# Kernel optimization log

Hardware: AMD Instinct MI355X
Metric: run time of the kernel (lower is better)

Reference implementation:

```python
import jax, jax.numpy as jnp
import numpy as np

B, Q, D = 8, 128, 2048
H, HD = 16, 128           # num_heads, head_dim (D == H*HD)
CACHE = 3968              # tokens already in KV cache; CACHE+Q == max_seq_len


def setup_inputs() -> dict:
    key = jax.random.key(0)
    ks = jax.random.split(key, 6)
    x = jax.random.normal(ks[0], (B, Q, D), dtype=jnp.float32)
    k_cache = jax.random.normal(ks[1], (B, H, CACHE, HD), dtype=jnp.float32)
    v_cache = jax.random.normal(ks[2], (B, H, CACHE, HD), dtype=jnp.float32)
    Wqkv = jax.random.normal(ks[3], (D, 3 * D), dtype=jnp.float32) * 0.02
    Wproj = jax.random.normal(ks[4], (D, D), dtype=jnp.float32) * 0.02
    bproj = jnp.zeros((D,), dtype=jnp.float32)
    return {"x": x, "k_cache": k_cache, "v_cache": v_cache,
            "Wqkv": Wqkv, "Wproj": Wproj, "bproj": bproj}


def reference(x, k_cache, v_cache, Wqkv, Wproj, bproj):
    # QKV projection (qkv_bias=False)
    qkv = x @ Wqkv                                   # [B, Q, 3D]
    qkv = qkv.reshape(B, Q, 3, H, HD)
    qkv = jnp.transpose(qkv, (2, 0, 3, 1, 4))        # [3, B, H, Q, HD]
    q, k_new, v_new = qkv[0], qkv[1], qkv[2]
    # KV-cache append (cache_pos + Q == max_seq_len, no roll)
    k_all = jnp.concatenate([k_cache, k_new], axis=2)  # [B, H, K, HD]
    v_all = jnp.concatenate([v_cache, v_new], axis=2)
    K = CACHE + Q
    scale = 1.0 / jnp.sqrt(jnp.float32(HD))
    scores = jnp.einsum('bhqd,bhkd->bhqk', q, k_all) * scale  # [B, H, Q, K]
    # Causal mask aligned to cache (bottom-right): query i sees keys j <= i + (K - Q)
    i = jnp.arange(Q)[:, None]
    j = jnp.arange(K)[None, :]
    mask = j > (i + (K - Q))
    scores = jnp.where(mask, jnp.float32(-jnp.inf), scores)
    attn = jax.nn.softmax(scores, axis=-1)
    out = jnp.einsum('bhqk,bhkd->bhqd', attn, v_all)   # [B, H, Q, HD]
    out = jnp.transpose(out, (0, 2, 1, 3)).reshape(B, Q, D)
    return out @ Wproj + bproj
```

## Files before the change

### kernel.cpp

```cpp
#include <hip/hip_runtime.h>

typedef unsigned int u32;
typedef unsigned short u16;
typedef short s16x8 __attribute__((ext_vector_type(8)));
typedef float f32x4 __attribute__((ext_vector_type(4)));

#define MFMA16(a,b,c) __builtin_amdgcn_mfma_f32_16x16x32_bf16((a),(b),(c),0,0,0)

#define Bb 8
#define Hh 16
#define Qq 128
#define HDd 128
#define Dd 2048
#define CACHE 3968
#define NSPLIT 8
#define SCALE 0.08838834764831845f
#define SM_OFF 8.0f

__device__ __forceinline__ u16 f2bf(float x){
  u32 u = __builtin_bit_cast(u32, x);
  u32 r = ((u >> 16) & 1u) + 0x7fffu;
  return (u16)((u + r) >> 16);
}
__device__ __forceinline__ float bf2f(u16 h){
  return __builtin_bit_cast(float, ((u32)h) << 16);
}
__device__ __forceinline__ u32 pk2(float a, float b){
  return (u32)f2bf(a) | ((u32)f2bf(b) << 16);
}
__device__ __forceinline__ u32 cvtpk(float a, float b){
  u32 r;
  asm("v_cvt_pk_bf16_f32 %0, %1, %2" : "=v"(r) : "v"(a), "v"(b));
  return r;
}
__device__ __forceinline__ float f4c(const float4& v, int j){
  return j==0 ? v.x : j==1 ? v.y : j==2 ? v.z : v.w;
}
__device__ __forceinline__ void gload_lds16(const void* g, void* l){
  __builtin_amdgcn_global_load_lds(
      (const __attribute__((address_space(1))) u32*)g,
      (__attribute__((address_space(3))) u32*)l, 16, 0, 0);
}
__device__ __forceinline__ void lgkm_barrier(){
  asm volatile("s_waitcnt lgkmcnt(0)" ::: "memory");
  __builtin_amdgcn_s_barrier();
}

__global__ void k_cvt(const float* __restrict__ s, u16* __restrict__ d, int n4){
  int i = blockIdx.x * 256 + threadIdx.x;
  if (i < n4){
    float4 v = *(const float4*)(s + (size_t)i * 4);
    *(uint2*)(d + (size_t)i * 4) = make_uint2(pk2(v.x, v.y), pk2(v.z, v.w));
  }
}

__global__ void k_tcvt(const float* __restrict__ s, u16* __restrict__ d, int R, int C){
  __shared__ float t[32][33];
  int tx = threadIdx.x & 31, ty = threadIdx.x >> 5;
  int c0 = blockIdx.x * 32, r0 = blockIdx.y * 32;
#pragma unroll
  for (int i = 0; i < 4; i++)
    t[ty + i*8][tx] = s[(size_t)(r0 + ty + i*8) * C + c0 + tx];
  __syncthreads();
#pragma unroll
  for (int i = 0; i < 4; i++)
    d[(size_t)(c0 + ty + i*8) * R + r0 + tx] = f2bf(t[tx][ty + i*8]);
}

template<int MODE>
__global__ __launch_bounds__(256)
void k_gemm(const u16* __restrict__ A, const u16* __restrict__ Bt, int K, int N,
            u16* __restrict__ oq, u16* __restrict__ ok, u16* __restrict__ ov,
            float* __restrict__ of, const float* __restrict__ bias)
{
  const int m0 = blockIdx.y * 128, n0 = blockIdx.x * 128;
  const int tid = threadIdx.x;
  const int w = tid >> 6, l = tid & 63;
  const int lg = l >> 4, lr = l & 15;
  const int wr = w >> 1, wc = w & 1;

  __shared__ u16 As[2][128 * 32];
  __shared__ u16 Bs[2][128 * 32];

  f32x4 acc[4][4];
#pragma unroll
  for (int i = 0; i < 4; i++)
#pragma unroll
    for (int j = 0; j < 4; j++) acc[i][j] = f32x4{0.f, 0.f, 0.f, 0.f};

  const int nt = K >> 5;

  auto stage = [&](int buf, int t){
    const int k0 = t << 5;
#pragma unroll
    for (int i = 0; i < 2; i++){
      int flat = i * 256 + tid;
      int row = flat >> 2, kq = flat & 3;
      const u16* ga = A + (size_t)(m0 + row) * K + k0 + kq * 8;
      gload_lds16(ga, (char*)&As[buf][0] + (size_t)(i*256 + w*64) * 16);
      const u16* gb = Bt + (size_t)(n0 + row) * K + k0 + kq * 8;
      gload_lds16(gb, (char*)&Bs[buf][0] + (size_t)(i*256 + w*64) * 16);
    }
  };

  stage(0, 0);
  asm volatile("s_waitcnt vmcnt(0)" ::: "memory");
  __syncthreads();

  for (int t = 0; t < nt; ++t){
    const int buf = t & 1;
    if (t + 1 < nt) stage(buf ^ 1, t + 1);
    s16x8 af[4], bfr[4];
#pragma unroll
    for (int i = 0; i < 4; i++){
      int row = wr*64 + i*16 + lr;
      af[i] = *(const s16x8*)&As[buf][row*32 + lg*8];
    }
#pragma unroll
    for (int j = 0; j < 4; j++){
      int col = wc*64 + j*16 + lr;
      bfr[j] = *(const s16x8*)&Bs[buf][col*32 + lg*8];
    }
#pragma unroll
    for (int i = 0; i < 4; i++)
#pragma unroll
      for (int j = 0; j < 4; j++)
        acc[i][j] = MFMA16(af[i], bfr[j], acc[i][j]);
    asm volatile("s_waitcnt vmcnt(0)" ::: "memory");
    __syncthreads();
  }

#pragma unroll
  for (int i = 0; i < 4; i++){
#pragma unroll
    for (int j = 0; j < 4; j++){
#pragma unroll
      for (int r = 0; r < 4; r++){
        int m = m0 + wr*64 + i*16 + lg*4 + r;
        int n = n0 + wc*64 + j*16 + lr;
        float v = acc[i][j][r];
        if (MODE == 0){
          int which = n >> 11;
          int h = (n >> 7) & 15, hd = n & 127;
          int b = m >> 7, qi = m & 127;
          size_t idx = (((size_t)(b * Hh + h)) * Qq + qi) * HDd + hd;
          if (which == 0)      oq[idx] = f2bf(v * SCALE);
          else if (which == 1) ok[idx] = f2bf(v);
          else                 ov[idx] = f2bf(v);
        } else {
          of[(size_t)m * N + n] = v + bias[n];
        }
      }
    }
  }
}

__global__ __launch_bounds__(512, 2)
void k_attn(const float* __restrict__ kc, const float* __restrict__ vc,
            const u16* __restrict__ qw, const u16* __restrict__ knw,
            const u16* __restrict__ vnw, float* __restrict__ opart,
            float2* __restrict__ ml)
{
  const int tid = threadIdx.x;
  const int w = tid >> 6, l = tid & 63;
  const int lg = l >> 4, lr = l & 15;

  __shared__ __align__(16) u16 Ks[2][64 * 136];
  __shared__ u32 Vts[2][128 * 32];

  const int rv = tid & 15, c4v = tid >> 4;

#pragma unroll 1
  for (int rep = 0; rep < 2; ++rep){
    const int vb = blockIdx.x * 2 + rep;
    const int bh = vb >> 3;
    const int sg = vb & 7;

    s16x8 qf[4];
    {
      const u16* qp = qw + (((size_t)bh * Qq + w*16 + lr) * HDd);
#pragma unroll
      for (int kk = 0; kk < 4; kk++) qf[kk] = *(const s16x8*)(qp + kk*32 + lg*8);
    }

    f32x4 acc[8];
#pragma unroll
    for (int i = 0; i < 8; i++) acc[i] = f32x4{0.f, 0.f, 0.f, 0.f};
    float lpart = 0.f;

    const float* kbase = kc + (size_t)bh * CACHE * HDd;
    const float* vbase = vc + (size_t)bh * CACHE * HDd;
    const u16* knb = knw + (size_t)bh * Qq * HDd;
    const u16* vnb = vnw + (size_t)bh * Qq * HDd;

    float4 kreg[4], vreg[4];

    auto loadc = [&](int c){
      if (c < 62){
#pragma unroll
        for (int i = 0; i < 4; i++){
          int flat = tid + i*512;
          int row = flat >> 5, c4 = flat & 31;
          kreg[i] = *(const float4*)(kbase + ((size_t)(c*64 + row)) * HDd + c4*4);
        }
#pragma unroll
        for (int a = 0; a < 4; a++)
          vreg[a] = *(const float4*)(vbase + ((size_t)(c*64 + rv + a*16)) * HDd + c4v*4);
      } else {
#pragma unroll
        for (int i = 0; i < 4; i++){
          int flat = tid + i*512;
          int row = flat >> 5, c4 = flat & 31;
          ushort4 u = *(const ushort4*)(knb + ((size_t)(c*64 + row - CACHE)) * HDd + c4*4);
          kreg[i] = make_float4(bf2f(u.x), bf2f(u.y), bf2f(u.z), bf2f(u.w));
        }
#pragma unroll
        for (int a = 0; a < 4; a++){
          ushort4 u = *(const ushort4*)(vnb + ((size_t)(c*64 + rv + a*16 - CACHE)) * HDd + c4v*4);
          vreg[a] = make_float4(bf2f(u.x), bf2f(u.y), bf2f(u.z), bf2f(u.w));
        }
      }
    };

    auto writeK = [&](int buf){
#pragma unroll
      for (int i = 0; i < 4; i++){
        int flat = tid + i*512;
        int row = flat >> 5, c4 = flat & 31;
        *(uint2*)&Ks[buf][row*136 + c4*4] =
            make_uint2(cvtpk(kreg[i].x, kreg[i].y), cvtpk(kreg[i].z, kreg[i].w));
      }
    };
    auto writeV = [&](int buf){
#pragma unroll
      for (int j = 0; j < 4; j++){
        int col = c4v*4 + j;
        int x2 = (col & 7) << 2;
        Vts[buf][col*32 + (rv ^ x2)]        = cvtpk(f4c(vreg[0], j), f4c(vreg[1], j));
        Vts[buf][col*32 + ((rv + 16) ^ x2)] = cvtpk(f4c(vreg[2], j), f4c(vreg[3], j));
      }
    };

    int cur = 0;
    loadc(sg * 8);
    writeK(0);
    writeV(0);
    __syncthreads();

    for (int cl = 0; cl < 8; ++cl){
      const int c = sg * 8 + cl;
      if (cl + 1 < 8) loadc(c + 1);

      f32x4 s[4];
      __builtin_amdgcn_s_setprio(1);
#pragma unroll
      for (int t = 0; t < 4; t++){
        s[t] = f32x4{0.f, 0.f, 0.f, 0.f};
        const u16* kp = &Ks[cur][(t*16 + lr) * 136];
#pragma unroll
        for (int kk = 0; kk < 4; kk++){
          s16x8 kf = *(const s16x8*)(kp + kk*32 + lg*8);
          s[t] = MFMA16(kf, qf[kk], s[t]);
        }
      }
      __builtin_amdgcn_s_setprio(0);

      if (c >= 62){
        int jn = c*64 - CACHE;
        int qi = w*16 + lr;
#pragma unroll
        for (int t = 0; t < 4; t++)
#pragma unroll
          for (int r = 0; r < 4; r++){
            int kn = jn + t*16 + lg*4 + r;
            if (kn > qi) s[t][r] = -__builtin_inff();
          }
      }

      float ps = 0.f;
#pragma unroll
      for (int t = 0; t < 4; t++)
#pragma unroll
        for (int r = 0; r < 4; r++){
          float p = __expf(s[t][r] - SM_OFF);
          s[t][r] = p;
          ps += p;
        }
      lpart += ps;

      s16x8 pf[2];
      {
        union { uint4 u; s16x8 v; } c0, c1;
        c0.u = make_uint4(cvtpk(s[0][0], s[1][0]), cvtpk(s[0][1], s[1][1]),
                          cvtpk(s[0][2], s[1][2]), cvtpk(s[0][3], s[1][3]));
        c1.u = make_uint4(cvtpk(s[2][0], s[3][0]), cvtpk(s[2][1], s[3][1]),
                          cvtpk(s[2][2], s[3][2]), cvtpk(s[2][3], s[3][3]));
        pf[0] = c0.v;
        pf[1] = c1.v;
      }

      if (cl + 1 < 8) writeK(cur ^ 1);

      __builtin_amdgcn_s_setprio(1);
#pragma unroll
      for (int t = 0; t < 8; t++){
        int col = t*16 + lr;
        const u32* vp = &Vts[cur][col * 32];
#pragma unroll
        for (int kk = 0; kk < 2; kk++){
          s16x8 vf = *(const s16x8*)(vp + ((16*kk + 4*lg) ^ ((col & 7) << 2)));
          acc[t] = MFMA16(vf, pf[kk], acc[t]);
        }
      }
      __builtin_amdgcn_s_setprio(0);

      if (cl + 1 < 8) writeV(cur ^ 1);

      lgkm_barrier();
      cur ^= 1;
    }

    float lsum = lpart;
    lsum += __shfl_xor(lsum, 16);
    lsum += __shfl_xor(lsum, 32);

    float* pbase = opart + (size_t)vb * (Qq * HDd);
    float* Lt = (float*)Ks;
#pragma unroll 1
    for (int half = 0; half < 2; half++){
      if ((w >> 2) == half){
        int ql = (w & 3) * 16 + lr;
#pragma unroll
        for (int t = 0; t < 8; t++)
#pragma unroll
          for (int r = 0; r < 4; r++)
            Lt[ql * 132 + t*16 + lg*4 + r] = acc[t][r];
      }
      __syncthreads();
      {
        int c32 = tid & 31;
#pragma unroll
        for (int j = 0; j < 4; j++){
          int ql = (tid >> 5) + j * 16;
          float4 v = *(const float4*)&Lt[ql * 132 + c32 * 4];
          *(float4*)&pbase[(size_t)(half * 64 + ql) * HDd + c32 * 4] = v;
        }
      }
      __syncthreads();
    }
    if (lg == 0)
      ml[(size_t)vb * Qq + w*16 + lr] = make_float2(SM_OFF, lsum);
    __syncthreads();
  }
}

__global__ __launch_bounds__(256)
void k_comb(const float* __restrict__ opart, const float2* __restrict__ ml,
            u16* __restrict__ ao)
{
  const int bh = blockIdx.x >> 2;
  const int q0 = (blockIdx.x & 3) * 32;
  const int tid = threadIdx.x;

  __shared__ float wgt[32][NSPLIT];
  __shared__ float Ls[32];

  {
    int row = tid >> 3, s = tid & 7;
    float2 v = ml[((size_t)(bh * NSPLIT + s)) * Qq + q0 + row];
    float m = v.x;
    m = fmaxf(m, __shfl_xor(m, 1));
    m = fmaxf(m, __shfl_xor(m, 2));
    m = fmaxf(m, __shfl_xor(m, 4));
    float e = __expf(v.x - m);
    float el = e * v.y;
    el += __shfl_xor(el, 1);
    el += __shfl_xor(el, 2);
    el += __shfl_xor(el, 4);
    wgt[row][s] = e;
    if (s == 0) Ls[row] = el;
  }
  __syncthreads();

  const int cp = tid & 63;
  const int r4 = tid >> 6;
  const int b = bh >> 4, h = bh & 15;
#pragma unroll
  for (int rr = 0; rr < 8; rr++){
    int row = r4 + rr*4;
    float2 a = make_float2(0.f, 0.f);
    const float* pb = opart + ((size_t)(bh * NSPLIT)) * (Qq * HDd)
                            + (size_t)(q0 + row) * HDd + cp*2;
#pragma unroll
    for (int s = 0; s < NSPLIT; s++){
      float2 p = *(const float2*)(pb + (size_t)s * (Qq * HDd));
      float wv = wgt[row][s];
      a.x += wv * p.x;
      a.y += wv * p.y;
    }
    float inv = 1.0f / Ls[row];
    u16* dst = ao + ((size_t)b * Qq + q0 + row) * Dd + h * HDd + cp*2;
    *(u32*)dst = pk2(a.x * inv, a.y * inv);
  }
}

extern "C" void kernel_launch(void* const* d_in, const int* in_sizes, int n_in,
                              void* d_out, int out_size, void* d_ws, size_t ws_size,
                              hipStream_t stream)
{
  const float* x     = (const float*)d_in[0];
  const float* kc    = (const float*)d_in[1];
  const float* vc    = (const float*)d_in[2];
  const float* wqkv  = (const float*)d_in[3];
  const float* wproj = (const float*)d_in[4];
  const float* bproj = (const float*)d_in[5];
  float* out = (float*)d_out;

  char* ws = (char*)d_ws;
  u16* xb  = (u16*)(ws);
  u16* wtq = (u16*)(ws + ((size_t)4  << 20));
  u16* wtp = (u16*)(ws + ((size_t)28 << 20));
  u16* qw  = (u16*)(ws + ((size_t)36 << 20));
  u16* knw = (u16*)(ws + ((size_t)40 << 20));
  u16* vnw = (u16*)(ws + ((size_t)44 << 20));
  u16* aow = (u16*)(ws + ((size_t)48 << 20));
  float* opart = (float*)(ws + ((size_t)52 << 20));
  float2* mlw  = (float2*)(ws + ((size_t)116 << 20));

  k_cvt<<<2048, 256, 0, stream>>>(x, xb, (1024 * 2048) / 4);
  k_tcvt<<<dim3(192, 64), 256, 0, stream>>>(wqkv, wtq, 2048, 6144);
  k_tcvt<<<dim3(64, 64), 256, 0, stream>>>(wproj, wtp, 2048, 2048);
  k_gemm<0><<<dim3(48, 8), 256, 0, stream>>>(xb, wtq, 2048, 6144,
                                             qw, knw, vnw, nullptr, nullptr);
  k_attn<<<512, 512, 0, stream>>>(kc, vc, qw, knw, vnw, opart, mlw);
  k_comb<<<Bb * Hh * 4, 256, 0, stream>>>(opart, mlw, aow);
  k_gemm<1><<<dim3(16, 8), 256, 0, stream>>>(aow, wtp, 2048, 2048,
                                             nullptr, nullptr, nullptr, out, bproj);
}
```

Before: 276.7 us.

## Halve attention split count and give each wave two query tiles

The attention kernel now uses 4 key splits per head with 256-thread blocks, and each wave handles 32 query rows instead of 16. Each K/V fragment read from shared memory feeds two MFMAs, which doubles reuse of LDS data per wave. Fewer splits also reduce the partial-output writes and the combine work. In exchange there are only 512 single-pass blocks, each register-heavier and with a longer serial loop over 16 chunks, so occupancy and the ability to hide memory latency may drop.

Result: slower. 403.5 us (+45.8%).

```diff
diff --git a/kernel.cpp b/kernel.cpp
--- a/kernel.cpp
+++ b/kernel.cpp
@@ -13,7 +13,7 @@
 #define HDd 128
 #define Dd 2048
 #define CACHE 3968
-#define NSPLIT 8
+#define NSPLIT 4
 #define SCALE 0.08838834764831845f
 #define SM_OFF 8.0f
 
@@ -155,7 +155,7 @@
   }
 }
 
-__global__ __launch_bounds__(512, 2)
+__global__ __launch_bounds__(256, 2)
 void k_attn(const float* __restrict__ kc, const float* __restrict__ vc,
             const u16* __restrict__ qw, const u16* __restrict__ knw,
             const u16* __restrict__ vnw, float* __restrict__ opart,
@@ -170,187 +170,210 @@
 
   const int rv = tid & 15, c4v = tid >> 4;
 
-#pragma unroll 1
-  for (int rep = 0; rep < 2; ++rep){
-    const int vb = blockIdx.x * 2 + rep;
-    const int bh = vb >> 3;
-    const int sg = vb & 7;
-
-    s16x8 qf[4];
-    {
-      const u16* qp = qw + (((size_t)bh * Qq + w*16 + lr) * HDd);
-#pragma unroll
-      for (int kk = 0; kk < 4; kk++) qf[kk] = *(const s16x8*)(qp + kk*32 + lg*8);
-    }
-
-    f32x4 acc[8];
-#pragma unroll
-    for (int i = 0; i < 8; i++) acc[i] = f32x4{0.f, 0.f, 0.f, 0.f};
-    float lpart = 0.f;
-
-    const float* kbase = kc + (size_t)bh * CACHE * HDd;
-    const float* vbase = vc + (size_t)bh * CACHE * HDd;
-    const u16* knb = knw + (size_t)bh * Qq * HDd;
-    const u16* vnb = vnw + (size_t)bh * Qq * HDd;
-
-    float4 kreg[4], vreg[4];
-
-    auto loadc = [&](int c){
-      if (c < 62){
-#pragma unroll
-        for (int i = 0; i < 4; i++){
-          int flat = tid + i*512;
-          int row = flat >> 5, c4 = flat & 31;
-          kreg[i] = *(const float4*)(kbase + ((size_t)(c*64 + row)) * HDd + c4*4);
+  const int vb = blockIdx.x;
+  const int bh = vb >> 2;
+  const int sg = vb & 3;
+
+  s16x8 qf[2][4];
+#pragma unroll
+  for (int u = 0; u < 2; u++){
+    const u16* qp = qw + (((size_t)bh * Qq + w*32 + u*16 + lr) * HDd);
+#pragma unroll
+    for (int kk = 0; kk < 4; kk++) qf[u][kk] = *(const s16x8*)(qp + kk*32 + lg*8);
+  }
+
+  f32x4 acc[2][8];
+#pragma unroll
+  for (int u = 0; u < 2; u++)
+#pragma unroll
+    for (int i = 0; i < 8; i++) acc[u][i] = f32x4{0.f, 0.f, 0.f, 0.f};
+  float lpart[2] = {0.f, 0.f};
+
+  const float* kbase = kc + (size_t)bh * CACHE * HDd;
+  const float* vbase = vc + (size_t)bh * CACHE * HDd;
+  const u16* knb = knw + (size_t)bh * Qq * HDd;
+  const u16* vnb = vnw + (size_t)bh * Qq * HDd;
+
+  float4 kreg[8], vreg[8];
+
+  auto loadc = [&](int c){
+    if (c < 62){
+#pragma unroll
+      for (int i = 0; i < 8; i++){
+        int flat = tid + i*256;
+        int row = flat >> 5, c4 = flat & 31;
+        kreg[i] = *(const float4*)(kbase + ((size_t)(c*64 + row)) * HDd + c4*4);
+      }
+#pragma unroll
+      for (int hh = 0; hh < 2; hh++)
+#pragma unroll
+        for (int a = 0; a < 4; a++)
+          vreg[hh*4+a] = *(const float4*)(vbase + ((size_t)(c*64 + rv + a*16)) * HDd
+                                          + (c4v + hh*16)*4);
+    } else {
+#pragma unroll
+      for (int i = 0; i < 8; i++){
+        int flat = tid + i*256;
+        int row = flat >> 5, c4 = flat & 31;
+        ushort4 u = *(const ushort4*)(knb + ((size_t)(c*64 + row - CACHE)) * HDd + c4*4);
+        kreg[i] = make_float4(bf2f(u.x), bf2f(u.y), bf2f(u.z), bf2f(u.w));
+      }
+#pragma unroll
+      for (int hh = 0; hh < 2; hh++)
+#pragma unroll
+        for (int a = 0; a < 4; a++){
+          ushort4 u = *(const ushort4*)(vnb + ((size_t)(c*64 + rv + a*16 - CACHE)) * HDd
+                                        + (c4v + hh*16)*4);
+          vreg[hh*4+a] = make_float4(bf2f(u.x), bf2f(u.y), bf2f(u.z), bf2f(u.w));
         }
-#pragma unroll
-        for (int a = 0; a < 4; a++)
-          vreg[a] = *(const float4*)(vbase + ((size_t)(c*64 + rv + a*16)) * HDd + c4v*4);
-      } else {
-#pragma unroll
-        for (int i = 0; i < 4; i++){
-          int flat = tid + i*512;
-          int row = flat >> 5, c4 = flat & 31;
-          ushort4 u = *(const ushort4*)(knb + ((size_t)(c*64 + row - CACHE)) * HDd + c4*4);
-          kreg[i] = make_float4(bf2f(u.x), bf2f(u.y), bf2f(u.z), bf2f(u.w));
-        }
-#pragma unroll
-        for (int a = 0; a < 4; a++){
-          ushort4 u = *(const ushort4*)(vnb + ((size_t)(c*64 + rv + a*16 - CACHE)) * HDd + c4v*4);
-          vreg[a] = make_float4(bf2f(u.x), bf2f(u.y), bf2f(u.z), bf2f(u.w));
-        }
-      }
-    };
-
-    auto writeK = [&](int buf){
-#pragma unroll
-      for (int i = 0; i < 4; i++){
-        int flat = tid + i*512;
-        int row = flat >> 5, c4 = flat & 31;
-        *(uint2*)&Ks[buf][row*136 + c4*4] =
-            make_uint2(cvtpk(kreg[i].x, kreg[i].y), cvtpk(kreg[i].z, kreg[i].w));
-      }
-    };
-    auto writeV = [&](int buf){
+    }
+  };
+
+  auto writeK = [&](int buf){
+#pragma unroll
+    for (int i = 0; i < 8; i++){
+      int flat = tid + i*256;
+      int row = flat >> 5, c4 = flat & 31;
+      *(uint2*)&Ks[buf][row*136 + c4*4] =
+          make_uint2(cvtpk(kreg[i].x, kreg[i].y), cvtpk(kreg[i].z, kreg[i].w));
+    }
+  };
+  auto writeV = [&](int buf){
+#pragma unroll
+    for (int hh = 0; hh < 2; hh++)
 #pragma unroll
       for (int j = 0; j < 4; j++){
-        int col = c4v*4 + j;
+        int col = (c4v + hh*16)*4 + j;
         int x2 = (col & 7) << 2;
-        Vts[buf][col*32 + (rv ^ x2)]        = cvtpk(f4c(vreg[0], j), f4c(vreg[1], j));
-        Vts[buf][col*32 + ((rv + 16) ^ x2)] = cvtpk(f4c(vreg[2], j), f4c(vreg[3], j));
-      }
-    };
-
-    int cur = 0;
-    loadc(sg * 8);
-    writeK(0);
-    writeV(0);
-    __syncthreads();
-
-    for (int cl = 0; cl < 8; ++cl){
-      const int c = sg * 8 + cl;
-      if (cl + 1 < 8) loadc(c + 1);
-
-      f32x4 s[4];
-      __builtin_amdgcn_s_setprio(1);
-#pragma unroll
-      for (int t = 0; t < 4; t++){
-        s[t] = f32x4{0.f, 0.f, 0.f, 0.f};
-        const u16* kp = &Ks[cur][(t*16 + lr) * 136];
-#pragma unroll
-        for (int kk = 0; kk < 4; kk++){
-          s16x8 kf = *(const s16x8*)(kp + kk*32 + lg*8);
-          s[t] = MFMA16(kf, qf[kk], s[t]);
-        }
-      }
-      __builtin_amdgcn_s_setprio(0);
-
-      if (c >= 62){
-        int jn = c*64 - CACHE;
-        int qi = w*16 + lr;
+        Vts[buf][col*32 + (rv ^ x2)]        = cvtpk(f4c(vreg[hh*4+0], j), f4c(vreg[hh*4+1], j));
+        Vts[buf][col*32 + ((rv + 16) ^ x2)] = cvtpk(f4c(vreg[hh*4+2], j), f4c(vreg[hh*4+3], j));
+      }
+  };
+
+  int cur = 0;
+  loadc(sg * 16);
+  writeK(0);
+  writeV(0);
+  __syncthreads();
+
+  for (int cl = 0; cl < 16; ++cl){
+    const int c = sg * 16 + cl;
+    if (cl + 1 < 16) loadc(c + 1);
+
+    f32x4 s[2][4];
+    __builtin_amdgcn_s_setprio(1);
+#pragma unroll
+    for (int t = 0; t < 4; t++){
+      s[0][t] = f32x4{0.f, 0.f, 0.f, 0.f};
+      s[1][t] = f32x4{0.f, 0.f, 0.f, 0.f};
+      const u16* kp = &Ks[cur][(t*16 + lr) * 136];
+#pragma unroll
+      for (int kk = 0; kk < 4; kk++){
+        s16x8 kf = *(const s16x8*)(kp + kk*32 + lg*8);
+        s[0][t] = MFMA16(kf, qf[0][kk], s[0][t]);
+        s[1][t] = MFMA16(kf, qf[1][kk], s[1][t]);
+      }
+    }
+    __builtin_amdgcn_s_setprio(0);
+
+    if (c >= 62){
+      int jn = c*64 - CACHE;
+#pragma unroll
+      for (int u = 0; u < 2; u++){
+        int qi = w*32 + u*16 + lr;
 #pragma unroll
         for (int t = 0; t < 4; t++)
 #pragma unroll
           for (int r = 0; r < 4; r++){
             int kn = jn + t*16 + lg*4 + r;
-            if (kn > qi) s[t][r] = -__builtin_inff();
+            if (kn > qi) s[u][t][r] = -__builtin_inff();
           }
       }
-
+    }
+
+    s16x8 pf[2][2];
+#pragma unroll
+    for (int u = 0; u < 2; u++){
       float ps = 0.f;
 #pragma unroll
       for (int t = 0; t < 4; t++)
 #pragma unroll
         for (int r = 0; r < 4; r++){
-          float p = __expf(s[t][r] - SM_OFF);
-          s[t][r] = p;
+          float p = __expf(s[u][t][r] - SM_OFF);
+          s[u][t][r] = p;
           ps += p;
         }
-      lpart += ps;
-
-      s16x8 pf[2];
-      {
-        union { uint4 u; s16x8 v; } c0, c1;
-        c0.u = make_uint4(cvtpk(s[0][0], s[1][0]), cvtpk(s[0][1], s[1][1]),
-                          cvtpk(s[0][2], s[1][2]), cvtpk(s[0][3], s[1][3]));
-        c1.u = make_uint4(cvtpk(s[2][0], s[3][0]), cvtpk(s[2][1], s[3][1]),
-                          cvtpk(s[2][2], s[3][2]), cvtpk(s[2][3], s[3][3]));
-        pf[0] = c0.v;
-        pf[1] = c1.v;
-      }
-
-      if (cl + 1 < 8) writeK(cur ^ 1);
-
-      __builtin_amdgcn_s_setprio(1);
-#pragma unroll
-      for (int t = 0; t < 8; t++){
-        int col = t*16 + lr;
-        const u32* vp = &Vts[cur][col * 32];
-#pragma unroll
-        for (int kk = 0; kk < 2; kk++){
-          s16x8 vf = *(const s16x8*)(vp + ((16*kk + 4*lg) ^ ((col & 7) << 2)));
-          acc[t] = MFMA16(vf, pf[kk], acc[t]);
-        }
-      }
-      __builtin_amdgcn_s_setprio(0);
-
-      if (cl + 1 < 8) writeV(cur ^ 1);
-
-      lgkm_barrier();
-      cur ^= 1;
-    }
-
-    float lsum = lpart;
-    lsum += __shfl_xor(lsum, 16);
-    lsum += __shfl_xor(lsum, 32);
-
-    float* pbase = opart + (size_t)vb * (Qq * HDd);
-    float* Lt = (float*)Ks;
+      lpart[u] += ps;
+      union { uint4 u4; s16x8 v; } c0, c1;
+      c0.u4 = make_uint4(cvtpk(s[u][0][0], s[u][1][0]), cvtpk(s[u][0][1], s[u][1][1]),
+                         cvtpk(s[u][0][2], s[u][1][2]), cvtpk(s[u][0][3], s[u][1][3]));
+      c1.u4 = make_uint4(cvtpk(s[u][2][0], s[u][3][0]), cvtpk(s[u][2][1], s[u][3][1]),
+                         cvtpk(s[u][2][2], s[u][3][2]), cvtpk(s[u][2][3], s[u][3][3]));
+      pf[u][0] = c0.v;
+      pf[u][1] = c1.v;
+    }
+
+    if (cl + 1 < 16) writeK(cur ^ 1);
+
+    __builtin_amdgcn_s_setprio(1);
+#pragma unroll
+    for (int t = 0; t < 8; t++){
+      int col = t*16 + lr;
+      const u32* vp = &Vts[cur][col * 32];
+#pragma unroll
+      for (int kk = 0; kk < 2; kk++){
+        s16x8 vf = *(const s16x8*)(vp + ((16*kk + 4*lg) ^ ((col & 7) << 2)));
+        acc[0][t] = MFMA16(vf, pf[0][kk], acc[0][t]);
+        acc[1][t] = MFMA16(vf, pf[1][kk], acc[1][t]);
+      }
+    }
+    __builtin_amdgcn_s_setprio(0);
+
+    if (cl + 1 < 16) writeV(cur ^ 1);
+
+    lgkm_barrier();
+    cur ^= 1;
+  }
+
+  float lsum[2];
+#pragma unroll
+  for (int u = 0; u < 2; u++){
+    lsum[u] = lpart[u];
+    lsum[u] += __shfl_xor(lsum[u], 16);
+    lsum[u] += __shfl_xor(lsum[u], 32);
+  }
+
+  float* pbase = opart + (size_t)vb * (Qq * HDd);
+  float* Lt = (float*)Ks;
 #pragma unroll 1
-    for (int half = 0; half < 2; half++){
-      if ((w >> 2) == half){
-        int ql = (w & 3) * 16 + lr;
+  for (int half = 0; half < 2; half++){
+    if ((w >> 1) == half){
+#pragma unroll
+      for (int u = 0; u < 2; u++){
+        int ql = (w & 1) * 32 + u*16 + lr;
 #pragma unroll
         for (int t = 0; t < 8; t++)
 #pragma unroll
           for (int r = 0; r < 4; r++)
-            Lt[ql * 132 + t*16 + lg*4 + r] = acc[t][r];
-      }
-      __syncthreads();
-      {
-        int c32 = tid & 31;
-#pragma unroll
-        for (int j = 0; j < 4; j++){
-          int ql = (tid >> 5) + j * 16;
-          float4 v = *(const float4*)&Lt[ql * 132 + c32 * 4];
-          *(float4*)&pbase[(size_t)(half * 64 + ql) * HDd + c32 * 4] = v;
-        }
-      }
-      __syncthreads();
-    }
-    if (lg == 0)
-      ml[(size_t)vb * Qq + w*16 + lr] = make_float2(SM_OFF, lsum);
+            Lt[ql * 132 + t*16 + lg*4 + r] = acc[u][t][r];
+      }
+    }
     __syncthreads();
+    {
+      int c32 = tid & 31;
+#pragma unroll
+      for (int j = 0; j < 8; j++){
+        int ql = (tid >> 5) + j * 8;
+        float4 v = *(const float4*)&Lt[ql * 132 + c32 * 4];
+        *(float4*)&pbase[(size_t)(half * 64 + ql) * HDd + c32 * 4] = v;
+      }
+    }
+    __syncthreads();
+  }
+  if (lg == 0){
+#pragma unroll
+    for (int u = 0; u < 2; u++)
+      ml[(size_t)vb * Qq + w*32 + u*16 + lr] = make_float2(SM_OFF, lsum[u]);
   }
 }
 
@@ -365,18 +388,16 @@
   __shared__ float wgt[32][NSPLIT];
   __shared__ float Ls[32];
 
-  {
-    int row = tid >> 3, s = tid & 7;
+  if (tid < 32 * NSPLIT){
+    int row = tid >> 2, s = tid & 3;
     float2 v = ml[((size_t)(bh * NSPLIT + s)) * Qq + q0 + row];
     float m = v.x;
     m = fmaxf(m, __shfl_xor(m, 1));
     m = fmaxf(m, __shfl_xor(m, 2));
-    m = fmaxf(m, __shfl_xor(m, 4));
     float e = __expf(v.x - m);
     float el = e * v.y;
     el += __shfl_xor(el, 1);
     el += __shfl_xor(el, 2);
-    el += __shfl_xor(el, 4);
     wgt[row][s] = e;
     if (s == 0) Ls[row] = el;
   }
@@ -432,7 +453,7 @@
   k_tcvt<<<dim3(64, 64), 256, 0, stream>>>(wproj, wtp, 2048, 2048);
   k_gemm<0><<<dim3(48, 8), 256, 0, stream>>>(xb, wtq, 2048, 6144,
                                              qw, knw, vnw, nullptr, nullptr);
-  k_attn<<<512, 512, 0, stream>>>(kc, vc, qw, knw, vnw, opart, mlw);
+  k_attn<<<Bb * Hh * NSPLIT, 256, 0, stream>>>(kc, vc, qw, knw, vnw, opart, mlw);
   k_comb<<<Bb * Hh * 4, 256, 0, stream>>>(opart, mlw, aow);
   k_gemm<1><<<dim3(16, 8), 256, 0, stream>>>(aow, wtp, 2048, 2048,
                                              nullptr, nullptr, nullptr, out, bproj);
```
